# Optimization experiments

Hardware: AMD Instinct MI355X
Metric: run time of the kernel (lower is better)

Reference implementation:

```python
import jax, jax.numpy as jnp
import numpy as np

HIDDEN = 768
FFN = 3072
E = 8
TOP_K = 2


def setup_inputs() -> dict:
    key = jax.random.key(0)
    k_x, k_r, k_w1, k_w2 = jax.random.split(key, 4)
    x = jax.random.normal(k_x, (1, 1024, HIDDEN), dtype=jnp.float32)
    # nn.Linear(hidden, E, bias=False): weight applied as x @ W^T; store as [H, E]
    bound = 1.0 / np.sqrt(HIDDEN)
    router_w = jax.random.uniform(k_r, (HIDDEN, E), minval=-bound, maxval=bound, dtype=jnp.float32)
    w1 = jax.random.normal(k_w1, (E, HIDDEN, FFN), dtype=jnp.float32) * 0.02
    w2 = jax.random.normal(k_w2, (E, FFN, HIDDEN), dtype=jnp.float32) * 0.02
    return {"x": x, "router_w": router_w, "w1": w1, "w2": w2}


def reference(x, router_w, w1, w2):
    B, T, H = x.shape
    xf = x.reshape(-1, H)                                  # [N, H]
    logits = xf @ router_w                                 # [N, E] (eval mode: no noise)
    probs = jax.nn.softmax(logits, axis=-1)
    top_v, top_i = jax.lax.top_k(probs, TOP_K)             # [N, K]
    top_v = top_v / jnp.sum(top_v, axis=-1, keepdims=True)  # renormalize top-k probs
    # Combine top-k weights into a dense per-expert gate; zero gates make the
    # dense per-expert computation mathematically identical to sparse dispatch.
    gates = jnp.sum(jax.nn.one_hot(top_i, E, dtype=xf.dtype) * top_v[..., None], axis=1)  # [N, E]
    h = jax.nn.gelu(jnp.einsum('nh,ehf->enf', xf, w1), approximate=False)  # [E, N, F]
    y = jnp.einsum('enf,efh->enh', h, w2)                  # [E, N, H]
    out = jnp.einsum('ne,enh->nh', gates, y)               # [N, H]
    return out.reshape(B, T, H)
```

## Files before the change

kernel.cpp:

```cpp
#include <hip/hip_runtime.h>
#include <cmath>

#define NTOK 1024
#define HD   768
#define FF   3072
#define NE   8
#define NSLOT (NTOK * 2)
#define BK   64

typedef unsigned short u16;
typedef unsigned int   u32;
typedef __bf16 bf16x8 __attribute__((ext_vector_type(8)));
typedef float  f32x4  __attribute__((ext_vector_type(4)));

__device__ __forceinline__ u16 f2bf(float f) {
  union { float f; u32 u; } v; v.f = f;
  u32 r = v.u + 0x7FFFu + ((v.u >> 16) & 1u);
  return (u16)(r >> 16);
}

__device__ __forceinline__ void load16(const void* g, void* l) {
  __builtin_amdgcn_global_load_lds(
      (const __attribute__((address_space(1))) u32*)g,
      (__attribute__((address_space(3))) u32*)l, 16, 0, 0);
}

__global__ __launch_bounds__(256) void convert_t_kernel(
    const float* __restrict__ src, u16* __restrict__ dst, int K, int N)
{
  const int e  = blockIdx.z;
  const int n0 = blockIdx.x * 64;
  const int k0 = blockIdx.y * 64;
  __shared__ u16 lt[64][65];
  const int tid = threadIdx.x;
  const int rr = tid >> 4;
  const int cc = (tid & 15) << 2;
  const float* s = src + (size_t)e * K * N;
#pragma unroll
  for (int j = 0; j < 4; ++j) {
    const int k = j * 16 + rr;
    const float4 v = *(const float4*)(s + (size_t)(k0 + k) * N + n0 + cc);
    lt[cc + 0][k] = f2bf(v.x); lt[cc + 1][k] = f2bf(v.y);
    lt[cc + 2][k] = f2bf(v.z); lt[cc + 3][k] = f2bf(v.w);
  }
  __syncthreads();
  u16* d = dst + (size_t)e * N * K;
#pragma unroll
  for (int j = 0; j < 4; ++j) {
    const int n = j * 16 + rr;
    ushort4 o;
    o.x = lt[n][cc]; o.y = lt[n][cc + 1]; o.z = lt[n][cc + 2]; o.w = lt[n][cc + 3];
    *(ushort4*)(d + (size_t)(n0 + n) * K + k0 + cc) = o;
  }
}

__global__ __launch_bounds__(256) void router_logits(
    const float* __restrict__ x, const float* __restrict__ rw,
    u16* __restrict__ xb, int* __restrict__ counts,
    int* __restrict__ ti, int* __restrict__ tpos, float* __restrict__ tg)
{
  __shared__ float rwt[NE * HD];
  const int tid = threadIdx.x;
  for (int i = tid; i < NE * HD; i += 256) {
    const int h = i >> 3, e = i & 7;
    rwt[e * HD + h] = rw[i];
  }
  __syncthreads();

  const int wid  = tid >> 6;
  const int lane = tid & 63;
  const int t    = blockIdx.x * 4 + wid;
  const float* xrow = x + (size_t)t * HD;
  u16* xbrow = xb + (size_t)t * HD;

  float acc[NE] = {};
#pragma unroll
  for (int j = 0; j < 12; ++j) {
    const int h = lane + j * 64;
    const float xv = xrow[h];
    xbrow[h] = f2bf(xv);
#pragma unroll
    for (int e = 0; e < NE; ++e) acc[e] += xv * rwt[e * HD + h];
  }
#pragma unroll
  for (int e = 0; e < NE; ++e) {
    float v = acc[e];
#pragma unroll
    for (int off = 32; off; off >>= 1) v += __shfl_down(v, off, 64);
    acc[e] = v;
  }

  if (lane == 0) {
    float v0 = -1e30f, v1 = -1e30f; int i0 = 0, i1 = 0;
#pragma unroll
    for (int e = 0; e < NE; ++e) {
      const float p = acc[e];
      if (p > v0) { v1 = v0; i1 = i0; v0 = p; i0 = e; }
      else if (p > v1) { v1 = p; i1 = e; }
    }
    const float e1 = expf(v1 - v0);
    const float g0 = 1.0f / (1.0f + e1);
    const float g1 = e1 / (1.0f + e1);
    const int p0 = atomicAdd(&counts[i0], 1);
    const int p1 = atomicAdd(&counts[i1], 1);
    ti[2 * t] = i0;  ti[2 * t + 1] = i1;
    tpos[2 * t] = p0; tpos[2 * t + 1] = p1;
    tg[2 * t] = g0;  tg[2 * t + 1] = g1;
  }
}

__global__ __launch_bounds__(1024) void router_scatter(
    const int* __restrict__ counts, const int* __restrict__ ti,
    const int* __restrict__ tpos, const float* __restrict__ tg,
    int* __restrict__ tos, float* __restrict__ gos, int* __restrict__ seg)
{
  __shared__ int offs[NE];
  const int t = threadIdx.x;
  if (t == 0) {
    int o = 0;
    for (int e = 0; e < NE; ++e) {
      offs[e] = o; seg[e] = o; seg[NE + e] = counts[e]; o += counts[e];
    }
  }
  __syncthreads();
  const int i0 = ti[2 * t], i1 = ti[2 * t + 1];
  const int s0 = offs[i0] + tpos[2 * t];
  const int s1 = offs[i1] + tpos[2 * t + 1];
  tos[s0] = t; gos[s0] = tg[2 * t];
  tos[s1] = t; gos[s1] = tg[2 * t + 1];
}


__global__ __launch_bounds__(256) void ffn1_kernel(
    const u16* __restrict__ xb, const u16* __restrict__ w1t,
    const int* __restrict__ tos, const int* __restrict__ seg,
    u16* __restrict__ hbuf)
{
  const int e   = blockIdx.z;
  const int cnt = seg[NE + e];
  const int m0  = blockIdx.y * 64;
  if (m0 >= cnt) return;
  const int start = seg[e];
  const int n0    = blockIdx.x * 64;

  __shared__ __align__(16) u16 As[64 * 64];
  __shared__ __align__(16) u16 Bs[64 * 64];
  __shared__ int toks[64];

  const int tid = threadIdx.x;
  if (tid < 64) toks[tid] = tos[start + min(m0 + tid, cnt - 1)];
  __syncthreads();

  const int lane = tid & 63;
  const int wid  = tid >> 6;

  const int r0 = wid * 8 + (lane >> 3);
  const int p  = lane & 7;
  const int c  = p ^ (r0 & 7);
  const u16* ag0 = xb + (size_t)toks[r0]      * HD + c * 8;
  const u16* ag1 = xb + (size_t)toks[r0 + 32] * HD + c * 8;
  const u16* bg0 = w1t + ((size_t)e * FF + n0 + r0)      * HD + c * 8;
  const u16* bg1 = w1t + ((size_t)e * FF + n0 + r0 + 32) * HD + c * 8;
  u16* al0 = As + (wid * 8) * 64;
  u16* al1 = As + (wid * 8 + 32) * 64;
  u16* bl0 = Bs + (wid * 8) * 64;
  u16* bl1 = Bs + (wid * 8 + 32) * 64;

  const int wm  = (wid >> 1) << 5;
  const int wn  = (wid & 1) << 5;
  const int q   = lane >> 4;
  const int r16 = lane & 15;

  f32x4 acc[2][2] = {};

  for (int k0 = 0; k0 < HD; k0 += BK) {
    load16(ag0 + k0, al0);
    load16(ag1 + k0, al1);
    load16(bg0 + k0, bl0);
    load16(bg1 + k0, bl1);
    __syncthreads();
#pragma unroll
    for (int s = 0; s < 2; ++s) {
      const int pa = ((s << 2) + q) ^ (r16 & 7);
      bf16x8 a0 = *(const bf16x8*)(&As[(wm + r16)      * 64 + (pa << 3)]);
      bf16x8 a1 = *(const bf16x8*)(&As[(wm + 16 + r16) * 64 + (pa << 3)]);
      bf16x8 b0 = *(const bf16x8*)(&Bs[(wn + r16)      * 64 + (pa << 3)]);
      bf16x8 b1 = *(const bf16x8*)(&Bs[(wn + 16 + r16) * 64 + (pa << 3)]);
      acc[0][0] = __builtin_amdgcn_mfma_f32_16x16x32_bf16(a0, b0, acc[0][0], 0, 0, 0);
      acc[0][1] = __builtin_amdgcn_mfma_f32_16x16x32_bf16(a0, b1, acc[0][1], 0, 0, 0);
      acc[1][0] = __builtin_amdgcn_mfma_f32_16x16x32_bf16(a1, b0, acc[1][0], 0, 0, 0);
      acc[1][1] = __builtin_amdgcn_mfma_f32_16x16x32_bf16(a1, b1, acc[1][1], 0, 0, 0);
    }
    __syncthreads();
  }

#pragma unroll
  for (int r = 0; r < 2; ++r) {
#pragma unroll
    for (int i = 0; i < 4; ++i) {
      const int mloc = wm + r * 16 + q * 4 + i;
      if (m0 + mloc < cnt) {
        u16* drow = hbuf + (size_t)(start + m0 + mloc) * FF + n0;
#pragma unroll
        for (int cix = 0; cix < 2; ++cix) {
          float v = acc[r][cix][i];
          v = 0.5f * v * (1.0f + erff(v * 0.70710678118f));
          drow[wn + cix * 16 + r16] = f2bf(v);
        }
      }
    }
  }
}

#define KSPLIT 2
#define KSEG   (FF / KSPLIT)

__global__ __launch_bounds__(256) void ffn2_kernel(
    const u16* __restrict__ hbuf, const u16* __restrict__ w2t,
    const int* __restrict__ tos, const float* __restrict__ gos,
    const int* __restrict__ seg, float* __restrict__ out)
{
  const int ez  = blockIdx.z;
  const int e   = ez >> 1;
  const int ks  = ez & 1;
  const int cnt = seg[NE + e];
  const int m0  = blockIdx.y * 64;
  if (m0 >= cnt) return;
  const int start = seg[e];
  const int n0    = blockIdx.x * 64;
  const int kbase = ks * KSEG;

  __shared__ __align__(16) u16 As[64 * 64];
  __shared__ __align__(16) u16 Bs[64 * 64];
  __shared__ int   toks[64];
  __shared__ float gates[64];

  const int tid = threadIdx.x;
  if (tid < 64) {
    const int idx = start + min(m0 + tid, cnt - 1);
    toks[tid]  = tos[idx];
    gates[tid] = gos[idx];
  }
  __syncthreads();

  const int lane = tid & 63;
  const int wid  = tid >> 6;

  const int r0 = wid * 8 + (lane >> 3);
  const int p  = lane & 7;
  const int c  = p ^ (r0 & 7);
  const u16* ag0 = hbuf + (size_t)(start + min(m0 + r0,      cnt - 1)) * FF + kbase + c * 8;
  const u16* ag1 = hbuf + (size_t)(start + min(m0 + r0 + 32, cnt - 1)) * FF + kbase + c * 8;
  const u16* bg0 = w2t + ((size_t)e * HD + n0 + r0)      * FF + kbase + c * 8;
  const u16* bg1 = w2t + ((size_t)e * HD + n0 + r0 + 32) * FF + kbase + c * 8;
  u16* al0 = As + (wid * 8) * 64;
  u16* al1 = As + (wid * 8 + 32) * 64;
  u16* bl0 = Bs + (wid * 8) * 64;
  u16* bl1 = Bs + (wid * 8 + 32) * 64;

  const int wm  = (wid >> 1) << 5;
  const int wn  = (wid & 1) << 5;
  const int q   = lane >> 4;
  const int r16 = lane & 15;

  f32x4 acc[2][2] = {};

  for (int k0 = 0; k0 < KSEG; k0 += BK) {
    load16(ag0 + k0, al0);
    load16(ag1 + k0, al1);
    load16(bg0 + k0, bl0);
    load16(bg1 + k0, bl1);
    __syncthreads();
#pragma unroll
    for (int s = 0; s < 2; ++s) {
      const int pa = ((s << 2) + q) ^ (r16 & 7);
      bf16x8 a0 = *(const bf16x8*)(&As[(wm + r16)      * 64 + (pa << 3)]);
      bf16x8 a1 = *(const bf16x8*)(&As[(wm + 16 + r16) * 64 + (pa << 3)]);
      bf16x8 b0 = *(const bf16x8*)(&Bs[(wn + r16)      * 64 + (pa << 3)]);
      bf16x8 b1 = *(const bf16x8*)(&Bs[(wn + 16 + r16) * 64 + (pa << 3)]);
      acc[0][0] = __builtin_amdgcn_mfma_f32_16x16x32_bf16(a0, b0, acc[0][0], 0, 0, 0);
      acc[0][1] = __builtin_amdgcn_mfma_f32_16x16x32_bf16(a0, b1, acc[0][1], 0, 0, 0);
      acc[1][0] = __builtin_amdgcn_mfma_f32_16x16x32_bf16(a1, b0, acc[1][0], 0, 0, 0);
      acc[1][1] = __builtin_amdgcn_mfma_f32_16x16x32_bf16(a1, b1, acc[1][1], 0, 0, 0);
    }
    __syncthreads();
  }

#pragma unroll
  for (int r = 0; r < 2; ++r) {
#pragma unroll
    for (int i = 0; i < 4; ++i) {
      const int mloc = wm + r * 16 + q * 4 + i;
      if (m0 + mloc < cnt) {
        const int tok  = toks[mloc];
        const float g  = gates[mloc];
        float* drow = out + (size_t)tok * HD + n0;
#pragma unroll
        for (int cix = 0; cix < 2; ++cix) {
          atomicAdd(drow + wn + cix * 16 + r16, g * acc[r][cix][i]);
        }
      }
    }
  }
}

extern "C" void kernel_launch(void* const* d_in, const int* in_sizes, int n_in,
                              void* d_out, int out_size, void* d_ws, size_t ws_size,
                              hipStream_t stream) {
  const float* x  = (const float*)d_in[0];
  const float* rw = (const float*)d_in[1];
  const float* w1 = (const float*)d_in[2];
  const float* w2 = (const float*)d_in[3];
  float* out = (float*)d_out;

  char* ws = (char*)d_ws;
  const size_t o_xb    = 0;
  const size_t o_hbuf  = o_xb + (size_t)NTOK * HD * 2;
  const size_t o_tos   = o_hbuf + (size_t)NSLOT * FF * 2;
  const size_t o_gos   = o_tos + (size_t)NSLOT * 4;
  const size_t o_seg   = o_gos + (size_t)NSLOT * 4;
  const size_t o_cnt   = o_seg + 64 * 4;
  const size_t o_ti    = o_cnt + NE * 4;
  const size_t o_tpos  = o_ti + (size_t)NSLOT * 4;
  const size_t o_tg    = o_tpos + (size_t)NSLOT * 4;
  const size_t o_w1t   = (o_tg + (size_t)NSLOT * 4 + 255) & ~(size_t)255;
  const size_t o_w2t   = o_w1t + (size_t)NE * HD * FF * 2;
  u16*   xb    = (u16*)(ws + o_xb);
  u16*   hbuf  = (u16*)(ws + o_hbuf);
  int*   tos   = (int*)(ws + o_tos);
  float* gos   = (float*)(ws + o_gos);
  int*   seg   = (int*)(ws + o_seg);
  int*   cnts  = (int*)(ws + o_cnt);
  int*   ti    = (int*)(ws + o_ti);
  int*   tpos  = (int*)(ws + o_tpos);
  float* tg    = (float*)(ws + o_tg);
  u16*   w1t   = (u16*)(ws + o_w1t);
  u16*   w2t   = (u16*)(ws + o_w2t);

  hipMemsetAsync(d_out, 0, (size_t)NTOK * HD * sizeof(float), stream);
  hipMemsetAsync(cnts, 0, NE * sizeof(int), stream);
  hipLaunchKernelGGL(convert_t_kernel, dim3(FF / 64, HD / 64, NE), dim3(256), 0, stream,
                     w1, w1t, HD, FF);
  hipLaunchKernelGGL(convert_t_kernel, dim3(HD / 64, FF / 64, NE), dim3(256), 0, stream,
                     w2, w2t, FF, HD);
  hipLaunchKernelGGL(router_logits, dim3(NTOK / 4), dim3(256), 0, stream,
                     x, rw, xb, cnts, ti, tpos, tg);
  hipLaunchKernelGGL(router_scatter, dim3(1), dim3(1024), 0, stream,
                     cnts, ti, tpos, tg, tos, gos, seg);
  hipLaunchKernelGGL(ffn1_kernel, dim3(FF / 64, NTOK / 64, NE), dim3(256), 0, stream,
                     xb, w1t, tos, seg, hbuf);
  hipLaunchKernelGGL(ffn2_kernel, dim3(HD / 64, NTOK / 64, NE * KSPLIT), dim3(256), 0, stream,
                     hbuf, w2t, tos, gos, seg, out);
}
```

Measured before the change: 279.6 us.

## Enlarge FFN GEMM tiles to 128x128, merge weight conversion launches, raise ffn2 K-split

Both expert GEMM kernels move from 64x64 to 128x128 output tiles, with each wave computing a 64x64 sub-tile (4x4 MFMA fragments). This cuts redundant LDS/global reloads of the A and B operands per FLOP. ffn2 raises its K-split from 2 to 4 to restore grid parallelism, at the cost of twice as many atomic adds into the output. The two weight-transpose launches are merged into one launch, which saves a kernel launch. Larger tiles raise register and LDS pressure and can waste work when an expert's token count is not a multiple of 128.

```diff
diff --git a/kernel.cpp b/kernel.cpp
--- a/kernel.cpp
+++ b/kernel.cpp
@@ -26,31 +26,36 @@
 }
 
 __global__ __launch_bounds__(256) void convert_t_kernel(
-    const float* __restrict__ src, u16* __restrict__ dst, int K, int N)
-{
-  const int e  = blockIdx.z;
-  const int n0 = blockIdx.x * 64;
-  const int k0 = blockIdx.y * 64;
+    const float* __restrict__ w1, const float* __restrict__ w2,
+    u16* __restrict__ w1t, u16* __restrict__ w2t)
+{
+  const int z = blockIdx.z;
+  const float* src; u16* dst; int K, N, n0, k0;
+  if (z < NE) {
+    src = w1 + (size_t)z * HD * FF; dst = w1t + (size_t)z * FF * HD;
+    K = HD; N = FF; n0 = blockIdx.x * 64; k0 = blockIdx.y * 64;
+  } else {
+    src = w2 + (size_t)(z - NE) * FF * HD; dst = w2t + (size_t)(z - NE) * HD * FF;
+    K = FF; N = HD; n0 = blockIdx.y * 64; k0 = blockIdx.x * 64;
+  }
   __shared__ u16 lt[64][65];
   const int tid = threadIdx.x;
   const int rr = tid >> 4;
   const int cc = (tid & 15) << 2;
-  const float* s = src + (size_t)e * K * N;
 #pragma unroll
   for (int j = 0; j < 4; ++j) {
     const int k = j * 16 + rr;
-    const float4 v = *(const float4*)(s + (size_t)(k0 + k) * N + n0 + cc);
+    const float4 v = *(const float4*)(src + (size_t)(k0 + k) * N + n0 + cc);
     lt[cc + 0][k] = f2bf(v.x); lt[cc + 1][k] = f2bf(v.y);
     lt[cc + 2][k] = f2bf(v.z); lt[cc + 3][k] = f2bf(v.w);
   }
   __syncthreads();
-  u16* d = dst + (size_t)e * N * K;
 #pragma unroll
   for (int j = 0; j < 4; ++j) {
     const int n = j * 16 + rr;
     ushort4 o;
     o.x = lt[n][cc]; o.y = lt[n][cc + 1]; o.z = lt[n][cc + 2]; o.w = lt[n][cc + 3];
-    *(ushort4*)(d + (size_t)(n0 + n) * K + k0 + cc) = o;
+    *(ushort4*)(dst + (size_t)(n0 + n) * K + k0 + cc) = o;
   }
 }
 
@@ -138,81 +143,87 @@
 {
   const int e   = blockIdx.z;
   const int cnt = seg[NE + e];
-  const int m0  = blockIdx.y * 64;
+  const int m0  = blockIdx.y * 128;
   if (m0 >= cnt) return;
   const int start = seg[e];
-  const int n0    = blockIdx.x * 64;
-
-  __shared__ __align__(16) u16 As[64 * 64];
-  __shared__ __align__(16) u16 Bs[64 * 64];
-  __shared__ int toks[64];
+  const int n0    = blockIdx.x * 128;
+
+  __shared__ __align__(16) u16 As[128 * 64];
+  __shared__ __align__(16) u16 Bs[128 * 64];
+  __shared__ int toks[128];
 
   const int tid = threadIdx.x;
-  if (tid < 64) toks[tid] = tos[start + min(m0 + tid, cnt - 1)];
+  if (tid < 128) toks[tid] = tos[start + min(m0 + tid, cnt - 1)];
   __syncthreads();
 
   const int lane = tid & 63;
   const int wid  = tid >> 6;
-
-  const int r0 = wid * 8 + (lane >> 3);
-  const int p  = lane & 7;
-  const int c  = p ^ (r0 & 7);
-  const u16* ag0 = xb + (size_t)toks[r0]      * HD + c * 8;
-  const u16* ag1 = xb + (size_t)toks[r0 + 32] * HD + c * 8;
-  const u16* bg0 = w1t + ((size_t)e * FF + n0 + r0)      * HD + c * 8;
-  const u16* bg1 = w1t + ((size_t)e * FF + n0 + r0 + 32) * HD + c * 8;
-  u16* al0 = As + (wid * 8) * 64;
-  u16* al1 = As + (wid * 8 + 32) * 64;
-  u16* bl0 = Bs + (wid * 8) * 64;
-  u16* bl1 = Bs + (wid * 8 + 32) * 64;
-
-  const int wm  = (wid >> 1) << 5;
-  const int wn  = (wid & 1) << 5;
+  const int rsub = lane >> 3;
+  const int c8   = (lane & 7) ^ rsub;
+
+  const u16* ag[4]; const u16* bg[4];
+  u16 *al[4], *bl[4];
+#pragma unroll
+  for (int i = 0; i < 4; ++i) {
+    const int rb = wid * 8 + i * 32;
+    ag[i] = xb + (size_t)toks[rb + rsub] * HD + c8 * 8;
+    bg[i] = w1t + ((size_t)e * FF + n0 + rb + rsub) * HD + c8 * 8;
+    al[i] = As + rb * 64;
+    bl[i] = Bs + rb * 64;
+  }
+
+  const int wm  = (wid >> 1) << 6;
+  const int wn  = (wid & 1) << 6;
   const int q   = lane >> 4;
   const int r16 = lane & 15;
 
-  f32x4 acc[2][2] = {};
+  f32x4 acc[4][4] = {};
 
   for (int k0 = 0; k0 < HD; k0 += BK) {
-    load16(ag0 + k0, al0);
-    load16(ag1 + k0, al1);
-    load16(bg0 + k0, bl0);
-    load16(bg1 + k0, bl1);
+#pragma unroll
+    for (int i = 0; i < 4; ++i) {
+      load16(ag[i] + k0, al[i]);
+      load16(bg[i] + k0, bl[i]);
+    }
     __syncthreads();
 #pragma unroll
     for (int s = 0; s < 2; ++s) {
       const int pa = ((s << 2) + q) ^ (r16 & 7);
-      bf16x8 a0 = *(const bf16x8*)(&As[(wm + r16)      * 64 + (pa << 3)]);
-      bf16x8 a1 = *(const bf16x8*)(&As[(wm + 16 + r16) * 64 + (pa << 3)]);
-      bf16x8 b0 = *(const bf16x8*)(&Bs[(wn + r16)      * 64 + (pa << 3)]);
-      bf16x8 b1 = *(const bf16x8*)(&Bs[(wn + 16 + r16) * 64 + (pa << 3)]);
-      acc[0][0] = __builtin_amdgcn_mfma_f32_16x16x32_bf16(a0, b0, acc[0][0], 0, 0, 0);
-      acc[0][1] = __builtin_amdgcn_mfma_f32_16x16x32_bf16(a0, b1, acc[0][1], 0, 0, 0);
-      acc[1][0] = __builtin_amdgcn_mfma_f32_16x16x32_bf16(a1, b0, acc[1][0], 0, 0, 0);
-      acc[1][1] = __builtin_amdgcn_mfma_f32_16x16x32_bf16(a1, b1, acc[1][1], 0, 0, 0);
+      bf16x8 af[4], bf[4];
+#pragma unroll
+      for (int t = 0; t < 4; ++t)
+        af[t] = *(const bf16x8*)(&As[(wm + t * 16 + r16) * 64 + pa * 8]);
+#pragma unroll
+      for (int t = 0; t < 4; ++t)
+        bf[t] = *(const bf16x8*)(&Bs[(wn + t * 16 + r16) * 64 + pa * 8]);
+#pragma unroll
+      for (int t = 0; t < 4; ++t)
+#pragma unroll
+        for (int c = 0; c < 4; ++c)
+          acc[t][c] = __builtin_amdgcn_mfma_f32_16x16x32_bf16(af[t], bf[c], acc[t][c], 0, 0, 0);
     }
     __syncthreads();
   }
 
 #pragma unroll
-  for (int r = 0; r < 2; ++r) {
+  for (int t = 0; t < 4; ++t) {
+    const int mbase = m0 + wm + t * 16 + q * 4;
 #pragma unroll
     for (int i = 0; i < 4; ++i) {
-      const int mloc = wm + r * 16 + q * 4 + i;
-      if (m0 + mloc < cnt) {
-        u16* drow = hbuf + (size_t)(start + m0 + mloc) * FF + n0;
-#pragma unroll
-        for (int cix = 0; cix < 2; ++cix) {
-          float v = acc[r][cix][i];
+      if (mbase + i < cnt) {
+        u16* drow = hbuf + (size_t)(start + mbase + i) * FF + n0 + wn;
+#pragma unroll
+        for (int c = 0; c < 4; ++c) {
+          float v = acc[t][c][i];
           v = 0.5f * v * (1.0f + erff(v * 0.70710678118f));
-          drow[wn + cix * 16 + r16] = f2bf(v);
+          drow[c * 16 + r16] = f2bf(v);
         }
       }
     }
   }
 }
 
-#define KSPLIT 2
+#define KSPLIT 4
 #define KSEG   (FF / KSPLIT)
 
 __global__ __launch_bounds__(256) void ffn2_kernel(
@@ -221,22 +232,22 @@
     const int* __restrict__ seg, float* __restrict__ out)
 {
   const int ez  = blockIdx.z;
-  const int e   = ez >> 1;
-  const int ks  = ez & 1;
+  const int e   = ez >> 2;
+  const int ks  = ez & 3;
   const int cnt = seg[NE + e];
-  const int m0  = blockIdx.y * 64;
+  const int m0  = blockIdx.y * 128;
   if (m0 >= cnt) return;
   const int start = seg[e];
-  const int n0    = blockIdx.x * 64;
+  const int n0    = blockIdx.x * 128;
   const int kbase = ks * KSEG;
 
-  __shared__ __align__(16) u16 As[64 * 64];
-  __shared__ __align__(16) u16 Bs[64 * 64];
-  __shared__ int   toks[64];
-  __shared__ float gates[64];
+  __shared__ __align__(16) u16 As[128 * 64];
+  __shared__ __align__(16) u16 Bs[128 * 64];
+  __shared__ int   toks[128];
+  __shared__ float gates[128];
 
   const int tid = threadIdx.x;
-  if (tid < 64) {
+  if (tid < 128) {
     const int idx = start + min(m0 + tid, cnt - 1);
     toks[tid]  = tos[idx];
     gates[tid] = gos[idx];
@@ -245,59 +256,66 @@
 
   const int lane = tid & 63;
   const int wid  = tid >> 6;
-
-  const int r0 = wid * 8 + (lane >> 3);
-  const int p  = lane & 7;
-  const int c  = p ^ (r0 & 7);
-  const u16* ag0 = hbuf + (size_t)(start + min(m0 + r0,      cnt - 1)) * FF + kbase + c * 8;
-  const u16* ag1 = hbuf + (size_t)(start + min(m0 + r0 + 32, cnt - 1)) * FF + kbase + c * 8;
-  const u16* bg0 = w2t + ((size_t)e * HD + n0 + r0)      * FF + kbase + c * 8;
-  const u16* bg1 = w2t + ((size_t)e * HD + n0 + r0 + 32) * FF + kbase + c * 8;
-  u16* al0 = As + (wid * 8) * 64;
-  u16* al1 = As + (wid * 8 + 32) * 64;
-  u16* bl0 = Bs + (wid * 8) * 64;
-  u16* bl1 = Bs + (wid * 8 + 32) * 64;
-
-  const int wm  = (wid >> 1) << 5;
-  const int wn  = (wid & 1) << 5;
+  const int rsub = lane >> 3;
+  const int c8   = (lane & 7) ^ rsub;
+
+  const u16* ag[4]; const u16* bg[4];
+  u16 *al[4], *bl[4];
+#pragma unroll
+  for (int i = 0; i < 4; ++i) {
+    const int rb = wid * 8 + i * 32;
+    ag[i] = hbuf + (size_t)(start + min(m0 + rb + rsub, cnt - 1)) * FF + kbase + c8 * 8;
+    bg[i] = w2t + ((size_t)e * HD + n0 + rb + rsub) * FF + kbase + c8 * 8;
+    al[i] = As + rb * 64;
+    bl[i] = Bs + rb * 64;
+  }
+
+  const int wm  = (wid >> 1) << 6;
+  const int wn  = (wid & 1) << 6;
   const int q   = lane >> 4;
   const int r16 = lane & 15;
 
-  f32x4 acc[2][2] = {};
+  f32x4 acc[4][4] = {};
 
   for (int k0 = 0; k0 < KSEG; k0 += BK) {
-    load16(ag0 + k0, al0);
-    load16(ag1 + k0, al1);
-    load16(bg0 + k0, bl0);
-    load16(bg1 + k0, bl1);
+#pragma unroll
+    for (int i = 0; i < 4; ++i) {
+      load16(ag[i] + k0, al[i]);
+      load16(bg[i] + k0, bl[i]);
+    }
     __syncthreads();
 #pragma unroll
     for (int s = 0; s < 2; ++s) {
       const int pa = ((s << 2) + q) ^ (r16 & 7);
-      bf16x8 a0 = *(const bf16x8*)(&As[(wm + r16)      * 64 + (pa << 3)]);
-      bf16x8 a1 = *(const bf16x8*)(&As[(wm + 16 + r16) * 64 + (pa << 3)]);
-      bf16x8 b0 = *(const bf16x8*)(&Bs[(wn + r16)      * 64 + (pa << 3)]);
-      bf16x8 b1 = *(const bf16x8*)(&Bs[(wn + 16 + r16) * 64 + (pa << 3)]);
-      acc[0][0] = __builtin_amdgcn_mfma_f32_16x16x32_bf16(a0, b0, acc[0][0], 0, 0, 0);
-      acc[0][1] = __builtin_amdgcn_mfma_f32_16x16x32_bf16(a0, b1, acc[0][1], 0, 0, 0);
-      acc[1][0] = __builtin_amdgcn_mfma_f32_16x16x32_bf16(a1, b0, acc[1][0], 0, 0, 0);
-      acc[1][1] = __builtin_amdgcn_mfma_f32_16x16x32_bf16(a1, b1, acc[1][1], 0, 0, 0);
+      bf16x8 af[4], bf[4];
+#pragma unroll
+      for (int t = 0; t < 4; ++t)
+        af[t] = *(const bf16x8*)(&As[(wm + t * 16 + r16) * 64 + pa * 8]);
+#pragma unroll
+      for (int t = 0; t < 4; ++t)
+        bf[t] = *(const bf16x8*)(&Bs[(wn + t * 16 + r16) * 64 + pa * 8]);
+#pragma unroll
+      for (int t = 0; t < 4; ++t)
+#pragma unroll
+        for (int c = 0; c < 4; ++c)
+          acc[t][c] = __builtin_amdgcn_mfma_f32_16x16x32_bf16(af[t], bf[c], acc[t][c], 0, 0, 0);
     }
     __syncthreads();
   }
 
 #pragma unroll
-  for (int r = 0; r < 2; ++r) {
+  for (int t = 0; t < 4; ++t) {
+    const int mbase = wm + t * 16 + q * 4;
 #pragma unroll
     for (int i = 0; i < 4; ++i) {
-      const int mloc = wm + r * 16 + q * 4 + i;
+      const int mloc = mbase + i;
       if (m0 + mloc < cnt) {
         const int tok  = toks[mloc];
         const float g  = gates[mloc];
-        float* drow = out + (size_t)tok * HD + n0;
-#pragma unroll
-        for (int cix = 0; cix < 2; ++cix) {
-          atomicAdd(drow + wn + cix * 16 + r16, g * acc[r][cix][i]);
+        float* drow = out + (size_t)tok * HD + n0 + wn;
+#pragma unroll
+        for (int c = 0; c < 4; ++c) {
+          atomicAdd(drow + c * 16 + r16, g * acc[t][c][i]);
         }
       }
     }
@@ -339,16 +357,14 @@
 
   hipMemsetAsync(d_out, 0, (size_t)NTOK * HD * sizeof(float), stream);
   hipMemsetAsync(cnts, 0, NE * sizeof(int), stream);
-  hipLaunchKernelGGL(convert_t_kernel, dim3(FF / 64, HD / 64, NE), dim3(256), 0, stream,
-                     w1, w1t, HD, FF);
-  hipLaunchKernelGGL(convert_t_kernel, dim3(HD / 64, FF / 64, NE), dim3(256), 0, stream,
-                     w2, w2t, FF, HD);
+  hipLaunchKernelGGL(convert_t_kernel, dim3(48, 12, 2 * NE), dim3(256), 0, stream,
+                     w1, w2, w1t, w2t);
   hipLaunchKernelGGL(router_logits, dim3(NTOK / 4), dim3(256), 0, stream,
                      x, rw, xb, cnts, ti, tpos, tg);
   hipLaunchKernelGGL(router_scatter, dim3(1), dim3(1024), 0, stream,
                      cnts, ti, tpos, tg, tos, gos, seg);
-  hipLaunchKernelGGL(ffn1_kernel, dim3(FF / 64, NTOK / 64, NE), dim3(256), 0, stream,
+  hipLaunchKernelGGL(ffn1_kernel, dim3(FF / 128, NTOK / 128, NE), dim3(256), 0, stream,
                      xb, w1t, tos, seg, hbuf);
-  hipLaunchKernelGGL(ffn2_kernel, dim3(HD / 64, NTOK / 64, NE * KSPLIT), dim3(256), 0, stream,
+  hipLaunchKernelGGL(ffn2_kernel, dim3(HD / 128, NTOK / 128, NE * KSPLIT), dim3(256), 0, stream,
                      hbuf, w2t, tos, gos, seg, out);
 }
```

Result: slower. 300.6 us (+7.5%).
